# Kernel tuning notes

Hardware: AMD Instinct MI355X
Metric: run time of the kernel (lower is better)

Reference implementation:

```python
import jax, jax.numpy as jnp
import numpy as np

G = 128          # voxel grid side
R = 2048         # rays
S = 128          # samples per ray
VD = 28          # 1 density + 27 SH coeffs (3 channels x 9)

# SH constants (match source module)
Y00 = 0.5 * np.sqrt(1.0 / np.pi)
H3 = 0.5 * np.sqrt(3.0 / np.pi)
H15 = 0.5 * np.sqrt(15.0 / np.pi)
Q5 = 0.25 * np.sqrt(5.0 / np.pi)
Q15 = 0.25 * np.sqrt(15.0 / np.pi)


def setup_inputs() -> dict:
    key = jax.random.key(0)
    k1, k2, k3, k4 = jax.random.split(key, 4)
    grid = jax.random.uniform(k1, (G, G, G, VD), dtype=jnp.float32)
    # continuous positions strictly inside the grid so all 8 corners are valid
    sample_positions = jax.random.uniform(k2, (R, S, 3), dtype=jnp.float32) * (G - 2)
    sample_distances = jax.random.uniform(k3, (R, S), dtype=jnp.float32) * 0.05
    ang = jax.random.uniform(k4, (R, 2), dtype=jnp.float32)
    viewing_angles = ang * jnp.array([np.pi, 2.0 * np.pi], dtype=jnp.float32)
    return {"grid": grid, "sample_positions": sample_positions,
            "sample_distances": sample_distances, "viewing_angles": viewing_angles}


def sh_basis(viewing_angles):
    # order matches harmonic(): [C00, Cm11, C01, C11, Cm22, Cm12, C02, C12, C22]
    th, ph = viewing_angles[:, 0], viewing_angles[:, 1]
    st, ct = jnp.sin(th), jnp.cos(th)
    sp, cp = jnp.sin(ph), jnp.cos(ph)
    return jnp.stack([
        jnp.full_like(th, Y00),          # Y_0_0
        H3 * st * sp,                    # Y_m1_1
        H3 * ct,                         # Y_0_1
        H3 * st * cp,                    # Y_1_1
        H15 * st * cp * st * sp,         # Y_m2_2
        H15 * st * sp * ct,              # Y_m1_2
        Q5 * (3.0 * ct * ct - 1.0),      # Y_0_2
        H15 * st * cp * ct,              # Y_1_2
        Q15 * ((st * cp) ** 2 - (st * sp) ** 2),  # Y_2_2
    ], axis=-1)  # [R, 9]


def trilinear(grid, pos):
    # pos: [R, S, 3] continuous coords -> [R, S, VD]
    p0 = jnp.floor(pos).astype(jnp.int32)
    fd = pos - p0.astype(pos.dtype)                  # fractional offsets (x_d, y_d, z_d)
    gmax = jnp.int32(grid.shape[0] - 1)
    out = jnp.zeros(pos.shape[:-1] + (grid.shape[-1],), dtype=grid.dtype)
    for dx in (0, 1):
        wx = fd[..., 0] if dx else (1.0 - fd[..., 0])
        for dy in (0, 1):
            wy = fd[..., 1] if dy else (1.0 - fd[..., 1])
            for dz in (0, 1):
                wz = fd[..., 2] if dz else (1.0 - fd[..., 2])
                ix = jnp.clip(p0[..., 0] + dx, 0, gmax)
                iy = jnp.clip(p0[..., 1] + dy, 0, gmax)
                iz = jnp.clip(p0[..., 2] + dz, 0, gmax)
                out = out + (wx * wy * wz)[..., None] * grid[ix, iy, iz]
    return out


def reference(grid, sample_positions, sample_distances, viewing_angles):
    feats = trilinear(grid, sample_positions)          # [R, S, 28]
    sigma = feats[..., 0]                              # [R, S]
    coeffs = feats[..., 1:].reshape(feats.shape[0], feats.shape[1], 3, 9)
    att = jnp.exp(-sigma * sample_distances)           # exp(-sigma_j * d_j)
    # Faithful to source: transmittance[i] = sum_{j<=i} exp(-sigma_j d_j)
    trans = jnp.cumsum(att, axis=1)                    # inclusive cumsum
    weight = trans * (1.0 - att)                       # [R, S]
    Y = sh_basis(viewing_angles)                       # [R, 9]
    rgb = jnp.einsum('rscn,rn->rsc', coeffs, Y)        # [R, S, 3]
    return jnp.sum(weight[..., None] * rgb, axis=1)    # [R, 3]
```

## Files before the change

### kernel.cpp

```cpp
#include <hip/hip_runtime.h>

#define GDIM 128
#define NS   128
#define VD   28

__global__ __launch_bounds__(512, 4) void plenoxel_kernel(
    const float* __restrict__ grid,
    const float* __restrict__ pos,
    const float* __restrict__ dist,
    const float* __restrict__ ang,
    float* __restrict__ out)
{
    const int r    = blockIdx.x;
    const int tid  = threadIdx.x;
    const int s    = tid >> 2;
    const int p    = tid & 3;
    const int dx   = p >> 1;
    const int dy   = p & 1;
    const int lane = tid & 63;
    const int wv   = tid >> 6;

    const float th = ang[2 * r + 0];
    const float ph = ang[2 * r + 1];
    float st, ct, sp, cp;
    sincosf(th, &st, &ct);
    sincosf(ph, &sp, &cp);
    const float Y00 = 0.28209479177387814f;
    const float H3  = 0.4886025119029199f;
    const float H15 = 1.0925484305920792f;
    const float Q5  = 0.31539156525252005f;
    const float Q15 = 0.5462742152960396f;
    float Y[9];
    Y[0] = Y00;
    Y[1] = H3 * st * sp;
    Y[2] = H3 * ct;
    Y[3] = H3 * st * cp;
    Y[4] = H15 * (st * cp) * (st * sp);
    Y[5] = H15 * (st * sp) * ct;
    Y[6] = Q5 * (3.f * ct * ct - 1.f);
    Y[7] = H15 * (st * cp) * ct;
    Y[8] = Q15 * ((st * cp) * (st * cp) - (st * sp) * (st * sp));

    const float* pp = pos + ((size_t)r * NS + s) * 3;
    const float x = pp[0], y = pp[1], z = pp[2];
    const float fx0 = floorf(x), fy0 = floorf(y), fz0 = floorf(z);
    const float fx = x - fx0, fy = y - fy0, fz = z - fz0;
    const int jx  = min(max((int)fx0 + dx, 0), GDIM - 1);
    const int jy  = min(max((int)fy0 + dy, 0), GDIM - 1);
    const int jz0 = min(max((int)fz0,      0), GDIM - 1);
    const int jz1 = min(max((int)fz0 + 1,  0), GDIM - 1);

    const float wxy = (dx ? fx : 1.f - fx) * (dy ? fy : 1.f - fy);
    const float wz0 = wxy * (1.f - fz);
    const float wz1 = wxy * fz;

    const float4* g0 = (const float4*)(grid + (((size_t)jx * GDIM + jy) * GDIM + jz0) * VD);
    const float4* g1 = (const float4*)(grid + (((size_t)jx * GDIM + jy) * GDIM + jz1) * VD);

    float f0[28], f1[28];
#pragma unroll
    for (int j = 0; j < 7; ++j) ((float4*)f0)[j] = g0[j];
#pragma unroll
    for (int j = 0; j < 7; ++j) ((float4*)f1)[j] = g1[j];

    float psig = wz0 * f0[0] + wz1 * f1[0];
    float d0r = 0.f, d0g = 0.f, d0b = 0.f;
    float d1r = 0.f, d1g = 0.f, d1b = 0.f;
#pragma unroll
    for (int n = 0; n < 9; ++n) {
        d0r += f0[1 + n]  * Y[n];
        d0g += f0[10 + n] * Y[n];
        d0b += f0[19 + n] * Y[n];
        d1r += f1[1 + n]  * Y[n];
        d1g += f1[10 + n] * Y[n];
        d1b += f1[19 + n] * Y[n];
    }
    float pr = wz0 * d0r + wz1 * d1r;
    float pg = wz0 * d0g + wz1 * d1g;
    float pb = wz0 * d0b + wz1 * d1b;

#pragma unroll
    for (int o = 1; o <= 2; o <<= 1) {
        psig += __shfl_xor(psig, (unsigned)o, 64);
        pr   += __shfl_xor(pr,   (unsigned)o, 64);
        pg   += __shfl_xor(pg,   (unsigned)o, 64);
        pb   += __shfl_xor(pb,   (unsigned)o, 64);
    }

    const float d   = dist[(size_t)r * NS + s];
    const float att = expf(-psig * d);

    float t = att;
#pragma unroll
    for (int o = 4; o < 64; o <<= 1) {
        const float v = __shfl_up(t, (unsigned)o, 64);
        if (lane >= o) t += v;
    }

    __shared__ float wave_sum[8];
    __shared__ float fin[8][3];
    if (lane == 63) wave_sum[wv] = t;
    __syncthreads();
    float carry = 0.f;
#pragma unroll
    for (int w = 0; w < 8; ++w) carry += (w < wv) ? wave_sum[w] : 0.f;

    const float trans  = t + carry;
    const float weight = trans * (1.f - att);

    const float m = (p == 0) ? weight : 0.f;
    float a0 = m * pr, a1 = m * pg, a2 = m * pb;
#pragma unroll
    for (int o = 4; o < 64; o <<= 1) {
        a0 += __shfl_xor(a0, (unsigned)o, 64);
        a1 += __shfl_xor(a1, (unsigned)o, 64);
        a2 += __shfl_xor(a2, (unsigned)o, 64);
    }
    if (lane == 0) { fin[wv][0] = a0; fin[wv][1] = a1; fin[wv][2] = a2; }
    __syncthreads();

    if (tid < 3) {
        float acc = 0.f;
#pragma unroll
        for (int w = 0; w < 8; ++w) acc += fin[w][tid];
        out[(size_t)r * 3 + tid] = acc;
    }
}

extern "C" void kernel_launch(void* const* d_in, const int* in_sizes, int n_in,
                              void* d_out, int out_size, void* d_ws, size_t ws_size,
                              hipStream_t stream) {
    const float* grid = (const float*)d_in[0];
    const float* pos  = (const float*)d_in[1];
    const float* dst  = (const float*)d_in[2];
    const float* ang  = (const float*)d_in[3];
    float* out = (float*)d_out;

    const int R = in_sizes[3] / 2;
    plenoxel_kernel<<<R, 512, 0, stream>>>(grid, pos, dst, ang, out);
}
```

Baseline: 370.4 us.

## Coalesce voxel gathers across quad threads by striping each z-column pair

Result: faster. 322.5 us (-13.0%).

```diff
diff --git a/kernel.cpp b/kernel.cpp
--- a/kernel.cpp
+++ b/kernel.cpp
@@ -3,6 +3,30 @@
 #define GDIM 128
 #define NS   128
 #define VD   28
+
+template<int P>
+__device__ __forceinline__ void accum_col(const float4* L, float wz0, float wz1,
+                                          const float* Y,
+                                          float& sg, float& rr, float& gg, float& bb)
+{
+#pragma unroll
+    for (int i = 0; i < 4; ++i) {
+        const float4 v = L[i];
+#pragma unroll
+        for (int k = 0; k < 4; ++k) {
+            const int c = 16 * i + 4 * P + k;
+            if (c < 56) {
+                const float f = (k == 0) ? v.x : (k == 1) ? v.y : (k == 2) ? v.z : v.w;
+                const float w = (c < 28) ? wz0 : wz1;
+                const int  ch = (c < 28) ? c : (c - 28);
+                if (ch == 0)       sg += w * f;
+                else if (ch < 10)  rr += (w * Y[ch - 1])  * f;
+                else if (ch < 19)  gg += (w * Y[ch - 10]) * f;
+                else               bb += (w * Y[ch - 19]) * f;
+            }
+        }
+    }
+}
 
 __global__ __launch_bounds__(512, 4) void plenoxel_kernel(
     const float* __restrict__ grid,
@@ -15,8 +39,6 @@
     const int tid  = threadIdx.x;
     const int s    = tid >> 2;
     const int p    = tid & 3;
-    const int dx   = p >> 1;
-    const int dy   = p & 1;
     const int lane = tid & 63;
     const int wv   = tid >> 6;
 
@@ -45,50 +67,60 @@
     const float x = pp[0], y = pp[1], z = pp[2];
     const float fx0 = floorf(x), fy0 = floorf(y), fz0 = floorf(z);
     const float fx = x - fx0, fy = y - fy0, fz = z - fz0;
-    const int jx  = min(max((int)fx0 + dx, 0), GDIM - 1);
-    const int jy  = min(max((int)fy0 + dy, 0), GDIM - 1);
-    const int jz0 = min(max((int)fz0,      0), GDIM - 1);
-    const int jz1 = min(max((int)fz0 + 1,  0), GDIM - 1);
+    const int jx0 = min(max((int)fx0,     0), GDIM - 1);
+    const int jx1 = min(max((int)fx0 + 1, 0), GDIM - 1);
+    const int jy0 = min(max((int)fy0,     0), GDIM - 1);
+    const int jy1 = min(max((int)fy0 + 1, 0), GDIM - 1);
+    const int jz0 = min(max((int)fz0,     0), GDIM - 2);
 
-    const float wxy = (dx ? fx : 1.f - fx) * (dy ? fy : 1.f - fy);
-    const float wz0 = wxy * (1.f - fz);
-    const float wz1 = wxy * fz;
+    const float* col[4];
+    col[0] = grid + (((size_t)jx0 * GDIM + jy0) * GDIM + jz0) * VD;
+    col[1] = grid + (((size_t)jx0 * GDIM + jy1) * GDIM + jz0) * VD;
+    col[2] = grid + (((size_t)jx1 * GDIM + jy0) * GDIM + jz0) * VD;
+    col[3] = grid + (((size_t)jx1 * GDIM + jy1) * GDIM + jz0) * VD;
+    const float wxy[4] = {(1.f - fx) * (1.f - fy), (1.f - fx) * fy,
+                          fx * (1.f - fy),         fx * fy};
+    float wza[4], wzb[4];
+#pragma unroll
+    for (int q = 0; q < 4; ++q) { wza[q] = wxy[q] * (1.f - fz); wzb[q] = wxy[q] * fz; }
 
-    const float4* g0 = (const float4*)(grid + (((size_t)jx * GDIM + jy) * GDIM + jz0) * VD);
-    const float4* g1 = (const float4*)(grid + (((size_t)jx * GDIM + jy) * GDIM + jz1) * VD);
+    float4 L[4][4];
+#pragma unroll
+    for (int q = 0; q < 4; ++q)
+#pragma unroll
+        for (int i = 0; i < 4; ++i)
+            L[q][i] = *(const float4*)(col[q] + 16 * i + 4 * p);
 
-    float f0[28], f1[28];
+    float sg = 0.f, rr = 0.f, gg = 0.f, bb = 0.f;
+    switch (p) {
+    case 0:
 #pragma unroll
-    for (int j = 0; j < 7; ++j) ((float4*)f0)[j] = g0[j];
+        for (int q = 0; q < 4; ++q) accum_col<0>(L[q], wza[q], wzb[q], Y, sg, rr, gg, bb);
+        break;
+    case 1:
 #pragma unroll
-    for (int j = 0; j < 7; ++j) ((float4*)f1)[j] = g1[j];
-
-    float psig = wz0 * f0[0] + wz1 * f1[0];
-    float d0r = 0.f, d0g = 0.f, d0b = 0.f;
-    float d1r = 0.f, d1g = 0.f, d1b = 0.f;
+        for (int q = 0; q < 4; ++q) accum_col<1>(L[q], wza[q], wzb[q], Y, sg, rr, gg, bb);
+        break;
+    case 2:
 #pragma unroll
-    for (int n = 0; n < 9; ++n) {
-        d0r += f0[1 + n]  * Y[n];
-        d0g += f0[10 + n] * Y[n];
-        d0b += f0[19 + n] * Y[n];
-        d1r += f1[1 + n]  * Y[n];
-        d1g += f1[10 + n] * Y[n];
-        d1b += f1[19 + n] * Y[n];
+        for (int q = 0; q < 4; ++q) accum_col<2>(L[q], wza[q], wzb[q], Y, sg, rr, gg, bb);
+        break;
+    default:
+#pragma unroll
+        for (int q = 0; q < 4; ++q) accum_col<3>(L[q], wza[q], wzb[q], Y, sg, rr, gg, bb);
+        break;
     }
-    float pr = wz0 * d0r + wz1 * d1r;
-    float pg = wz0 * d0g + wz1 * d1g;
-    float pb = wz0 * d0b + wz1 * d1b;
 
 #pragma unroll
     for (int o = 1; o <= 2; o <<= 1) {
-        psig += __shfl_xor(psig, (unsigned)o, 64);
-        pr   += __shfl_xor(pr,   (unsigned)o, 64);
-        pg   += __shfl_xor(pg,   (unsigned)o, 64);
-        pb   += __shfl_xor(pb,   (unsigned)o, 64);
+        sg += __shfl_xor(sg, (unsigned)o, 64);
+        rr += __shfl_xor(rr, (unsigned)o, 64);
+        gg += __shfl_xor(gg, (unsigned)o, 64);
+        bb += __shfl_xor(bb, (unsigned)o, 64);
     }
 
     const float d   = dist[(size_t)r * NS + s];
-    const float att = expf(-psig * d);
+    const float att = expf(-sg * d);
 
     float t = att;
 #pragma unroll
@@ -109,7 +141,7 @@
     const float weight = trans * (1.f - att);
 
     const float m = (p == 0) ? weight : 0.f;
-    float a0 = m * pr, a1 = m * pg, a2 = m * pb;
+    float a0 = m * rr, a1 = m * gg, a2 = m * bb;
 #pragma unroll
     for (int o = 4; o < 64; o <<= 1) {
         a0 += __shfl_xor(a0, (unsigned)o, 64);
```
